# Kernel tuning notes

Hardware: AMD Instinct MI355X
Metric: run time of the kernel (lower is better)

## Reference

```python
import jax, jax.numpy as jnp
import numpy as np

N_NODES = 50000
N_EDGES = 800000
DIMS = [128, 512, 256, 128]
EPS = 1e-5


def setup_inputs() -> dict:
    key = jax.random.key(0)
    ks = jax.random.split(key, 2 + 5 * 3)
    inp = {
        "x": jax.random.normal(ks[0], (N_NODES, DIMS[0]), dtype=jnp.float32),
        "edge_index": jax.random.randint(ks[1], (2, N_EDGES), 0, N_NODES, dtype=jnp.int64),
    }
    ki = 2
    for i in range(3):
        din, dout = DIMS[i], DIMS[i + 1]
        s = 1.0 / np.sqrt(din)
        inp[f"Wl{i}"] = jax.random.uniform(ks[ki + 0], (din, dout), jnp.float32, -s, s)
        inp[f"bl{i}"] = jax.random.uniform(ks[ki + 1], (dout,), jnp.float32, -s, s)
        inp[f"Wr{i}"] = jax.random.uniform(ks[ki + 2], (din, dout), jnp.float32, -s, s)
        inp[f"g{i}"] = jnp.ones((dout,), jnp.float32)
        inp[f"b{i}"] = jnp.zeros((dout,), jnp.float32)
        ki += 5
    return inp


def _sage_mean(x, src, dst, Wl, bl, Wr):
    n = x.shape[0]
    agg = jax.ops.segment_sum(x[src], dst, num_segments=n)  # [N, din]
    deg = jax.ops.segment_sum(jnp.ones((src.shape[0],), x.dtype), dst, num_segments=n)
    mean = agg / jnp.maximum(deg, 1.0)[:, None]
    return mean @ Wl + bl + x @ Wr


def _bn(h, gamma, beta):
    m = h.mean(axis=0)
    v = h.var(axis=0)
    return gamma * (h - m) * jax.lax.rsqrt(v + EPS) + beta


def reference(x, edge_index, Wl0, bl0, Wr0, g0, b0, Wl1, bl1, Wr1, g1, b1, Wl2, bl2, Wr2, g2, b2):
    src, dst = edge_index[0], edge_index[1]
    params = [(Wl0, bl0, Wr0, g0, b0), (Wl1, bl1, Wr1, g1, b1), (Wl2, bl2, Wr2, g2, b2)]
    h = x
    for Wl, bl, Wr, g, b in params:
        h = _sage_mean(h, src, dst, Wl, bl, Wr)
        h = _bn(h, g, b)
        h = jax.nn.relu(h)
        # dropout: identity in eval mode
    return h
```

## Files before the change

### kernel.cpp

```cpp
#include <hip/hip_runtime.h>
#include <cstdint>
#include <cstddef>


#define EPS_BN 1e-5f

typedef unsigned short ushort_t;
typedef __attribute__((ext_vector_type(8))) short short8;
typedef __attribute__((ext_vector_type(4))) float float4v;
typedef __attribute__((ext_vector_type(2))) float float2v;
typedef __attribute__((ext_vector_type(2))) unsigned int uint2v;
typedef __attribute__((ext_vector_type(4))) unsigned int uint4v;

__device__ __forceinline__ float bflo(unsigned int w) {
    union { unsigned int i; float f; } v; v.i = w << 16; return v.f;
}
__device__ __forceinline__ float bfhi(unsigned int w) {
    union { unsigned int i; float f; } v; v.i = w & 0xffff0000u; return v.f;
}
__device__ __forceinline__ ushort_t f2bf(float f) {
    union { float f; unsigned int i; } v; v.f = f;
    unsigned int r = v.i + 0x7fffu + ((v.i >> 16) & 1u);
    return (ushort_t)(r >> 16);
}

__device__ __forceinline__ void async_copy16(void* lds, const void* g) {
    __builtin_amdgcn_global_load_lds(
        (const __attribute__((address_space(1))) unsigned int*)g,
        (__attribute__((address_space(3))) unsigned int*)lds, 16, 0, 0);
}

__device__ __forceinline__ void edge_sd(const int* __restrict__ p, int e, int ne,
                                        bool is64, int& s, int& d) {
    if (is64) { s = p[2 * e];  d = p[2 * ne + 2 * e]; }
    else      { s = p[e];      d = p[ne + e]; }
}
__device__ __forceinline__ int edge_d(const int* __restrict__ p, int e, int ne, bool is64) {
    return is64 ? p[2 * ne + 2 * e] : p[ne + e];
}

__device__ __forceinline__ bool detect_is64(const int* __restrict__ edges,
                                            int* sh_flag, int t) {
    if (t == 0) *sh_flag = 1;
    __syncthreads();
    if (t < 64 && edges[2 * t + 1] != 0) *sh_flag = 0;
    __syncthreads();
    return *sh_flag != 0;
}

#define EPB 2048

__global__ __launch_bounds__(256) void bhist_kernel(
    const int* __restrict__ edges, int ne, int* __restrict__ gcnt) {
    __shared__ int h[256];
    __shared__ int f64;
    int t = threadIdx.x;
    bool is64 = detect_is64(edges, &f64, t);
    h[t] = 0;
    __syncthreads();
    int base_e = blockIdx.x * EPB;
    #pragma unroll
    for (int u = 0; u < EPB / 256; ++u) {
        int i = base_e + u * 256 + t;
        if (i < ne) atomicAdd(&h[edge_d(edges, i, ne, is64) >> 8], 1);
    }
    __syncthreads();
    if (h[t]) atomicAdd(&gcnt[t], h[t]);
}

__global__ __launch_bounds__(256) void bscan_kernel(
    const int* __restrict__ gcnt, int nb, int ne,
    int* __restrict__ bbase, int* __restrict__ bcur) {
    __shared__ int sh[256];
    int t = threadIdx.x;
    int v = (t < nb) ? gcnt[t] : 0;
    sh[t] = v;
    __syncthreads();
    for (int o = 1; o < 256; o <<= 1) {
        int x = (t >= o) ? sh[t - o] : 0;
        __syncthreads();
        sh[t] += x;
        __syncthreads();
    }
    int excl = sh[t] - v;
    if (t < nb) { bbase[t] = excl; bcur[t] = excl; }
    if (t == nb) bbase[t] = ne;
    if (t == 0 && nb == 256) bbase[256] = ne;
}

__global__ __launch_bounds__(256) void bscatter_kernel(
    const int* __restrict__ edges, int ne,
    int* __restrict__ bcur, int* __restrict__ packed) {
    __shared__ int h[256];
    __shared__ int chunkb[256];
    __shared__ int lcur[256];
    __shared__ int f64;
    int t = threadIdx.x;
    bool is64 = detect_is64(edges, &f64, t);
    h[t] = 0;
    lcur[t] = 0;
    __syncthreads();
    int base_e = blockIdx.x * EPB;
    int ent[EPB / 256], eb[EPB / 256];
    #pragma unroll
    for (int u = 0; u < EPB / 256; ++u) {
        int i = base_e + u * 256 + t;
        if (i < ne) {
            int s, d;
            edge_sd(edges, i, ne, is64, s, d);
            ent[u] = s | ((d & 255) << 24);
            eb[u] = d >> 8;
            atomicAdd(&h[eb[u]], 1);
        } else eb[u] = -1;
    }
    __syncthreads();
    if (h[t]) chunkb[t] = atomicAdd(&bcur[t], h[t]);
    __syncthreads();
    #pragma unroll
    for (int u = 0; u < EPB / 256; ++u) {
        if (eb[u] >= 0) {
            int lp = atomicAdd(&lcur[eb[u]], 1);
            packed[chunkb[eb[u]] + lp] = ent[u];
        }
    }
}

__global__ __launch_bounds__(256) void bbuild_kernel(
    const int* __restrict__ packed, const int* __restrict__ bbase,
    int* __restrict__ rowptr, int* __restrict__ csr_src, int n) {
    __shared__ int h[256];
    __shared__ int cur[256];
    int t = threadIdx.x;
    int bb = blockIdx.x;
    int base = bbase[bb], cnt = bbase[bb + 1] - base;
    h[t] = 0;
    __syncthreads();
    for (int i = t; i < cnt; i += 256)
        atomicAdd(&h[(unsigned)packed[base + i] >> 24], 1);
    __syncthreads();
    int v = h[t];
    for (int o = 1; o < 256; o <<= 1) {
        int x = (t >= o) ? h[t - o] : 0;
        __syncthreads();
        h[t] += x;
        __syncthreads();
    }
    int excl = h[t] - v;
    int node = bb * 256 + t;
    if (node <= n) rowptr[node] = base + excl;
    cur[t] = excl;
    __syncthreads();
    for (int i = t; i < cnt; i += 256) {
        int e = packed[base + i];
        int lp = atomicAdd(&cur[(unsigned)e >> 24], 1);
        csr_src[base + lp] = e & 0xffffff;
    }
}

__global__ void prep_all_kernel(
    const float* __restrict__ x, ushort_t* __restrict__ xb, int nxb,
    const float* __restrict__ Wl0, const float* __restrict__ Wr0,
    ushort_t* __restrict__ WT0, int nb0,
    const float* __restrict__ Wl1, const float* __restrict__ Wr1,
    ushort_t* __restrict__ WT1c, int nb1,
    const float* __restrict__ Wl2, const float* __restrict__ Wr2,
    ushort_t* __restrict__ WT2c) {
    const int D0 = 128, D1 = 512, D2 = 256, D3 = 128;
    int b = blockIdx.x;
    if (b < nxb) {
        int i = b * 256 + threadIdx.x;
        xb[i] = f2bf(x[i]);
        return;
    }
    b -= nxb;
    if (b < nb0) {
        int idx = b * 256 + threadIdx.x;
        int K2 = 2 * D0;
        int nn = idx / K2, k = idx - nn * K2;
        float v = (k < D0) ? Wl0[(size_t)k * D1 + nn] : Wr0[(size_t)(k - D0) * D1 + nn];
        WT0[idx] = f2bf(v);
        return;
    }
    b -= nb0;
    if (b < nb1) {
        int idx = b * 256 + threadIdx.x;
        int nn = idx / D1, k = idx - nn * D1;
        float v = (nn < D2) ? Wl1[(size_t)k * D2 + nn] : Wr1[(size_t)k * D2 + (nn - D2)];
        WT1c[idx] = f2bf(v);
        return;
    }
    b -= nb1;
    {
        int idx = b * 256 + threadIdx.x;
        int nn = idx / D2, k = idx - nn * D2;
        float v = (nn < D3) ? Wl2[(size_t)k * D3 + nn] : Wr2[(size_t)k * D3 + (nn - D3)];
        WT2c[idx] = f2bf(v);
    }
}

template <int VEC> struct VecT;
template <> struct VecT<2> { using T = unsigned int; };
template <> struct VecT<4> { using T = uint2v; };
template <> struct VecT<8> { using T = uint4v; };

template <int VEC>
__device__ __forceinline__ void vunpack(typename VecT<VEC>::T v, unsigned int* w) {
    if constexpr (VEC == 2) { w[0] = v; }
    else if constexpr (VEC == 4) { w[0] = v.x; w[1] = v.y; }
    else { w[0] = v.x; w[1] = v.y; w[2] = v.z; w[3] = v.w; }
}

template <int VEC>
__device__ __forceinline__ void vaccum(typename VecT<VEC>::T v, float* acc) {
    unsigned int w[VEC / 2];
    vunpack<VEC>(v, w);
    #pragma unroll
    for (int i = 0; i < VEC / 2; ++i) {
        acc[2 * i + 0] += bflo(w[i]);
        acc[2 * i + 1] += bfhi(w[i]);
    }
}

template <int VEC>
__device__ __forceinline__ void gather_sum(
    const ushort_t* __restrict__ base, const int* __restrict__ csr_src,
    int e0, int e1, int rstride, float* acc) {
    using VT = typename VecT<VEC>::T;
    int e = e0;
    for (; e + 16 <= e1; e += 16) {
        VT v[16];
        #pragma unroll
        for (int u = 0; u < 16; ++u)
            v[u] = *(const VT*)(base + (size_t)csr_src[e + u] * rstride);
        #pragma unroll
        for (int u = 0; u < 16; ++u) vaccum<VEC>(v[u], acc);
    }
    if (e + 8 <= e1) {
        VT v[8];
        #pragma unroll
        for (int u = 0; u < 8; ++u)
            v[u] = *(const VT*)(base + (size_t)csr_src[e + u] * rstride);
        #pragma unroll
        for (int u = 0; u < 8; ++u) vaccum<VEC>(v[u], acc);
        e += 8;
    }
    if (e + 4 <= e1) {
        VT v[4];
        #pragma unroll
        for (int u = 0; u < 4; ++u)
            v[u] = *(const VT*)(base + (size_t)csr_src[e + u] * rstride);
        #pragma unroll
        for (int u = 0; u < 4; ++u) vaccum<VEC>(v[u], acc);
        e += 4;
    }
    if (e + 2 <= e1) {
        VT v0 = *(const VT*)(base + (size_t)csr_src[e] * rstride);
        VT v1 = *(const VT*)(base + (size_t)csr_src[e + 1] * rstride);
        vaccum<VEC>(v0, acc); vaccum<VEC>(v1, acc);
        e += 2;
    }
    if (e < e1)
        vaccum<VEC>(*(const VT*)(base + (size_t)csr_src[e] * rstride), acc);
}

template <int VEC>
__global__ __launch_bounds__(256) void aggregate_wave_kernel(
    const ushort_t* __restrict__ h, ushort_t* __restrict__ mean,
    const int* __restrict__ rowptr, const int* __restrict__ csr_src, int nnodes) {
    const int din = VEC * 64;
    const int wave = threadIdx.x >> 6;
    const int lane = threadIdx.x & 63;
    const int wstride = gridDim.x * 4;
    using VT = typename VecT<VEC>::T;
    for (int wid = blockIdx.x * 4 + wave; wid < nnodes; wid += wstride) {
        int e0 = rowptr[wid], e1 = rowptr[wid + 1];
        float acc[VEC];
        #pragma unroll
        for (int i = 0; i < VEC; ++i) acc[i] = 0.f;
        gather_sum<VEC>(h + (size_t)lane * VEC, csr_src, e0, e1, din, acc);

        int deg = e1 - e0;
        float scale = 1.0f / (float)(deg > 1 ? deg : 1);
        unsigned int o[VEC / 2];
        #pragma unroll
        for (int i = 0; i < VEC / 2; ++i)
            o[i] = (unsigned int)f2bf(acc[2 * i] * scale) |
                   ((unsigned int)f2bf(acc[2 * i + 1] * scale) << 16);
        VT ov;
        if constexpr (VEC == 2) { ov = o[0]; }
        else if constexpr (VEC == 4) { ov.x = o[0]; ov.y = o[1]; }
        else { ov.x = o[0]; ov.y = o[1]; ov.z = o[2]; ov.w = o[3]; }
        *(VT*)(mean + (size_t)wid * din + (size_t)lane * VEC) = ov;
    }
}

template <int VEC>
__global__ __launch_bounds__(256) void aggregate_add_kernel(
    const ushort_t* __restrict__ PR, const float* __restrict__ bias,
    ushort_t* __restrict__ pre,
    const int* __restrict__ rowptr, const int* __restrict__ csr_src, int nnodes,
    float* __restrict__ gsum, float* __restrict__ gsq) {
    const int D = VEC * 64;
    const int stride = 2 * D;
    __shared__ float s_red[2][4][VEC * 64];
    const int wave = threadIdx.x >> 6;
    const int lane = threadIdx.x & 63;
    const int wstride = gridDim.x * 4;
    using VT = typename VecT<VEC>::T;

    float ssum[VEC], ssq[VEC];
    #pragma unroll
    for (int i = 0; i < VEC; ++i) { ssum[i] = 0.f; ssq[i] = 0.f; }

    for (int wid = blockIdx.x * 4 + wave; wid < nnodes; wid += wstride) {
        int e0 = rowptr[wid], e1 = rowptr[wid + 1];
        float acc[VEC];
        #pragma unroll
        for (int i = 0; i < VEC; ++i) acc[i] = 0.f;
        gather_sum<VEC>(PR + (size_t)lane * VEC, csr_src, e0, e1, stride, acc);

        int deg = e1 - e0;
        float scale = 1.0f / (float)(deg > 1 ? deg : 1);

        VT rv = *(const VT*)(PR + (size_t)wid * stride + D + (size_t)lane * VEC);
        unsigned int rw[VEC / 2];
        vunpack<VEC>(rv, rw);
        float o[VEC];
        #pragma unroll
        for (int i = 0; i < VEC / 2; ++i) {
            o[2 * i + 0] = bflo(rw[i]);
            o[2 * i + 1] = bfhi(rw[i]);
        }
        #pragma unroll
        for (int i = 0; i < VEC; ++i) {
            o[i] += acc[i] * scale + bias[lane * VEC + i];
            ssum[i] += o[i];
            ssq[i] += o[i] * o[i];
        }

        unsigned int ow[VEC / 2];
        #pragma unroll
        for (int i = 0; i < VEC / 2; ++i)
            ow[i] = (unsigned int)f2bf(o[2 * i]) | ((unsigned int)f2bf(o[2 * i + 1]) << 16);
        VT ov;
        if constexpr (VEC == 2) { ov = ow[0]; }
        else if constexpr (VEC == 4) { ov.x = ow[0]; ov.y = ow[1]; }
        else { ov.x = ow[0]; ov.y = ow[1]; ov.z = ow[2]; ov.w = ow[3]; }
        *(VT*)(pre + (size_t)wid * D + (size_t)lane * VEC) = ov;
    }

    #pragma unroll
    for (int i = 0; i < VEC; ++i) {
        s_red[0][wave][lane * VEC + i] = ssum[i];
        s_red[1][wave][lane * VEC + i] = ssq[i];
    }
    __syncthreads();
    int t = threadIdx.x;
    if (t < D) {
        float a = s_red[0][0][t] + s_red[0][1][t] + s_red[0][2][t] + s_red[0][3][t];
        float q = s_red[1][0][t] + s_red[1][1][t] + s_red[1][2][t] + s_red[1][3][t];
        atomicAdd(&gsum[t], a);
        atomicAdd(&gsq[t], q);
    }
}

template <bool DUAL, bool BIAS, bool STATS>
__global__ __launch_bounds__(256, 4) void gemm_glds_kernel(
    const ushort_t* __restrict__ A1, const ushort_t* __restrict__ A2,
    const ushort_t* __restrict__ BT, const float* __restrict__ bias,
    ushort_t* __restrict__ Cb, int N, int K1, int Ktot, int Wtot, int nxShift,
    float* __restrict__ gsum, float* __restrict__ gsq) {
    __shared__ ushort_t As[2 * 128 * 32];
    __shared__ ushort_t Bs[2 * 128 * 32];

    const int tid = threadIdx.x;
    const int wave = tid >> 6;
    const int lane = tid & 63;
    const int quad = lane >> 4;
    const int l15 = lane & 15;
    const int sw3 = l15 & 3;

    const int nwg = gridDim.x;
    const int q = nwg >> 3, rr = nwg & 7;
    const int o = blockIdx.x;
    const int xcd = o & 7, sub = o >> 3;
    const int wgid = (xcd < rr ? xcd * (q + 1) : rr * (q + 1) + (xcd - rr) * q) + sub;
    const int bx = wgid & ((1 << nxShift) - 1);
    const int by = wgid >> nxShift;

    const int rowBase = by * 128;
    const int colBase = bx * 128;
    const int wm = (wave >> 1) * 64;
    const int wn = (wave & 1) * 64;

    float4v acc[4][4];
    #pragma unroll
    for (int i = 0; i < 4; ++i)
        #pragma unroll
        for (int j = 0; j < 4; ++j)
            acc[i][j] = (float4v){0.f, 0.f, 0.f, 0.f};

    const int nkt = Ktot / 32;
    const int khalf = K1 / 32;

    auto stage = [&](int buf, int kt) {
        const ushort_t* Asrc = A1;
        int kg = kt * 32;
        if (DUAL && kt >= khalf) { Asrc = A2; kg = (kt - khalf) * 32; }
        const int kb = kt * 32;
        #pragma unroll
        for (int u = 0; u < 2; ++u) {
            int c = u * 256 + tid;
            int r = c >> 2, cc = c & 3;
            int off = (cc ^ (r & 3)) * 8;
            int grow = rowBase + r;
            if (grow >= N) grow = N - 1;
            async_copy16(&As[buf * 4096 + c * 8], Asrc + (size_t)grow * K1 + kg + off);
        }
        #pragma unroll
        for (int u = 0; u < 2; ++u) {
            int c = u * 256 + tid;
            int r = c >> 2, cc = c & 3;
            int off = (cc ^ (r & 3)) * 8;
            async_copy16(&Bs[buf * 4096 + c * 8], BT + (size_t)(colBase + r) * Ktot + kb + off);
        }
    };

    stage(0, 0);
    int cur = 0;
    for (int kt = 0; kt < nkt; ++kt) {
        if (kt + 1 < nkt) {
            stage(cur ^ 1, kt + 1);
            asm volatile("s_waitcnt vmcnt(4)\n\ts_barrier" ::: "memory");
        } else {
            asm volatile("s_waitcnt vmcnt(0)\n\ts_barrier" ::: "memory");
        }

        short8 af[4], bf4[4];
        #pragma unroll
        for (int i = 0; i < 4; ++i)
            af[i] = *(const short8*)&As[cur * 4096 + (wm + i * 16 + l15) * 32 + (quad ^ sw3) * 8];
        #pragma unroll
        for (int j = 0; j < 4; ++j)
            bf4[j] = *(const short8*)&Bs[cur * 4096 + (wn + j * 16 + l15) * 32 + (quad ^ sw3) * 8];
        __builtin_amdgcn_s_setprio(1);
        #pragma unroll
        for (int i = 0; i < 4; ++i)
            #pragma unroll
            for (int j = 0; j < 4; ++j)
                acc[i][j] = __builtin_amdgcn_mfma_f32_16x16x32_bf16(bf4[j], af[i], acc[i][j], 0, 0, 0);
        __builtin_amdgcn_s_setprio(0);
        asm volatile("s_barrier" ::: "memory");
        cur ^= 1;
    }

    float cs[4][4], cq[4][4];
    if constexpr (STATS) {
        #pragma unroll
        for (int j = 0; j < 4; ++j)
            #pragma unroll
            for (int r = 0; r < 4; ++r) { cs[j][r] = 0.f; cq[j][r] = 0.f; }
    }

    ushort_t* lws = &As[wave * 2048];
    #pragma unroll
    for (int p = 0; p < 2; ++p) {
        #pragma unroll
        for (int jj = 0; jj < 2; ++jj) {
            int j = 2 * p + jj;
            float4 bv = make_float4(0.f, 0.f, 0.f, 0.f);
            if (BIAS) bv = *(const float4*)(bias + colBase + wn + j * 16 + quad * 4);
            #pragma unroll
            for (int i = 0; i < 4; ++i) {
                float v0 = acc[i][j][0] + bv.x;
                float v1 = acc[i][j][1] + bv.y;
                float v2 = acc[i][j][2] + bv.z;
                float v3 = acc[i][j][3] + bv.w;
                if constexpr (STATS) {
                    if (rowBase + wm + i * 16 + l15 < N) {
                        cs[j][0] += v0; cq[j][0] += v0 * v0;
                        cs[j][1] += v1; cq[j][1] += v1 * v1;
                        cs[j][2] += v2; cq[j][2] += v2 * v2;
                        cs[j][3] += v3; cq[j][3] += v3 * v3;
                    }
                }
                uint2 pk;
                pk.x = (unsigned int)f2bf(v0) | ((unsigned int)f2bf(v1) << 16);
                pk.y = (unsigned int)f2bf(v2) | ((unsigned int)f2bf(v3) << 16);
                *(uint2*)&lws[(i * 16 + l15) * 32 + jj * 16 + quad * 4] = pk;
            }
        }
        __syncthreads();
        #pragma unroll
        for (int it = 0; it < 4; ++it) {
            int c = it * 64 + lane;
            int row = c >> 2, coff = (c & 3) * 8;
            int grow = rowBase + wm + row;
            if (grow < N) {
                uint4 v = *(const uint4*)&lws[row * 32 + coff];
                *(uint4*)(Cb + (size_t)grow * Wtot + colBase + wn + p * 32 + coff) = v;
            }
        }
        __syncthreads();
    }

    if constexpr (STATS) {
        #pragma unroll
        for (int j = 0; j < 4; ++j)
            #pragma unroll
            for (int r = 0; r < 4; ++r) {
                #pragma unroll
                for (int m = 1; m < 16; m <<= 1) {
                    cs[j][r] += __shfl_xor(cs[j][r], m);
                    cq[j][r] += __shfl_xor(cq[j][r], m);
                }
            }
        if (l15 == 0) {
            #pragma unroll
            for (int j = 0; j < 4; ++j)
                #pragma unroll
                for (int r = 0; r < 4; ++r) {
                    int col = colBase + wn + j * 16 + quad * 4 + r;
                    atomicAdd(&gsum[col], cs[j][r]);
                    atomicAdd(&gsq[col], cq[j][r]);
                }
        }
    }
}

__global__ void bn_relu_b2b_kernel(const ushort_t* __restrict__ h, ushort_t* __restrict__ hb,
                                   int N, int D,
                                   const float* __restrict__ sum, const float* __restrict__ sumsq,
                                   const float* __restrict__ g, const float* __restrict__ b) {
    size_t idx = (size_t)blockIdx.x * blockDim.x + threadIdx.x;
    size_t tot = (size_t)N * D / 2;
    if (idx >= tot) return;
    int cp = (int)(idx & (size_t)(D / 2 - 1));
    int c0 = cp * 2, c1 = c0 + 1;
    float m0 = sum[c0] / (float)N, m1 = sum[c1] / (float)N;
    float i0 = rsqrtf(sumsq[c0] / (float)N - m0 * m0 + EPS_BN);
    float i1 = rsqrtf(sumsq[c1] / (float)N - m1 * m1 + EPS_BN);
    unsigned int w = ((const unsigned int*)h)[idx];
    float v0 = g[c0] * (bflo(w) - m0) * i0 + b[c0];
    float v1 = g[c1] * (bfhi(w) - m1) * i1 + b[c1];
    v0 = v0 > 0.f ? v0 : 0.f;
    v1 = v1 > 0.f ? v1 : 0.f;
    ((unsigned int*)hb)[idx] = (unsigned int)f2bf(v0) | ((unsigned int)f2bf(v1) << 16);
}

__global__ void bn_relu_b2f_kernel(const ushort_t* __restrict__ h, float* __restrict__ hf,
                                   int N, int D,
                                   const float* __restrict__ sum, const float* __restrict__ sumsq,
                                   const float* __restrict__ g, const float* __restrict__ b) {
    size_t idx = (size_t)blockIdx.x * blockDim.x + threadIdx.x;
    size_t tot = (size_t)N * D / 2;
    if (idx >= tot) return;
    int cp = (int)(idx & (size_t)(D / 2 - 1));
    int c0 = cp * 2, c1 = c0 + 1;
    float m0 = sum[c0] / (float)N, m1 = sum[c1] / (float)N;
    float i0 = rsqrtf(sumsq[c0] / (float)N - m0 * m0 + EPS_BN);
    float i1 = rsqrtf(sumsq[c1] / (float)N - m1 * m1 + EPS_BN);
    unsigned int w = ((const unsigned int*)h)[idx];
    float v0 = g[c0] * (bflo(w) - m0) * i0 + b[c0];
    float v1 = g[c1] * (bfhi(w) - m1) * i1 + b[c1];
    float2v o;
    o.x = v0 > 0.f ? v0 : 0.f;
    o.y = v1 > 0.f ? v1 : 0.f;
    *(float2v*)(hf + idx * 2) = o;
}

extern "C" void kernel_launch(void* const* d_in, const int* in_sizes, int n_in,
                              void* d_out, int out_size, void* d_ws, size_t ws_size,
                              hipStream_t stream) {
    const float* x     = (const float*)d_in[0];
    const int*   edges = (const int*)d_in[1];
    const float* Wl0 = (const float*)d_in[2];
    const float* bl0 = (const float*)d_in[3];
    const float* Wr0 = (const float*)d_in[4];
    const float* g0  = (const float*)d_in[5];
    const float* b0  = (const float*)d_in[6];
    const float* Wl1 = (const float*)d_in[7];
    const float* bl1 = (const float*)d_in[8];
    const float* Wr1 = (const float*)d_in[9];
    const float* g1  = (const float*)d_in[10];
    const float* b1  = (const float*)d_in[11];
    const float* Wl2 = (const float*)d_in[12];
    const float* bl2 = (const float*)d_in[13];
    const float* Wr2 = (const float*)d_in[14];
    const float* g2  = (const float*)d_in[15];
    const float* b2  = (const float*)d_in[16];

    const int D0 = 128, D1 = 512, D2 = 256, D3 = 128;
    const int n  = in_sizes[0] / D0;
    const int ne = in_sizes[1] / 2;
    const int NB = (n + 255) >> 8;

    char* base = (char*)d_ws;
    size_t off = 0;
    auto alloc = [&](size_t bytes) -> char* {
        char* p = base + off;
        off = (off + bytes + 255) & ~(size_t)255;
        return p;
    };
    int*      gcnt    = (int*)alloc(256 * 4);
    float*    stats   = (float*)alloc(6 * 512 * 4);
    size_t    zero_span = off;
    int*      bbase   = (int*)alloc(257 * 4);
    int*      bcur    = (int*)alloc(256 * 4);
    int*      packed  = (int*)alloc((size_t)ne * 4);
    int*      rowptr  = (int*)alloc((size_t)(n + 1) * 4);
    int*      csr_src = (int*)alloc((size_t)ne * 4);
    ushort_t* xb      = (ushort_t*)alloc((size_t)n * D0 * 2);
    ushort_t* mb      = (ushort_t*)alloc((size_t)n * 512 * 2);
    ushort_t* h1b     = (ushort_t*)alloc((size_t)n * D1 * 2);
    ushort_t* h2b     = (ushort_t*)alloc((size_t)n * D2 * 2);
    ushort_t* hpre    = (ushort_t*)alloc((size_t)n * 512 * 2);
    ushort_t* WT0     = (ushort_t*)alloc((size_t)D1 * 2 * D0 * 2);
    ushort_t* WT1c    = (ushort_t*)alloc((size_t)(2 * D2) * D1 * 2);
    ushort_t* WT2c    = (ushort_t*)alloc((size_t)(2 * D3) * D2 * 2);
    float*    out     = (float*)d_out;
    (void)ws_size; (void)n_in; (void)out_size;

    hipMemsetAsync(base, 0, zero_span, stream);

    int ablk = (ne + EPB - 1) / EPB;
    bhist_kernel<<<ablk, 256, 0, stream>>>(edges, ne, gcnt);
    bscan_kernel<<<1, 256, 0, stream>>>(gcnt, NB, ne, bbase, bcur);
    bscatter_kernel<<<ablk, 256, 0, stream>>>(edges, ne, bcur, packed);
    bbuild_kernel<<<NB, 256, 0, stream>>>(packed, bbase, rowptr, csr_src, n);

    const int nxb = (n * D0) / 256;
    const int nb0 = (D1 * 2 * D0) / 256;
    const int nb1 = (2 * D2 * D1) / 256;
    const int nb2 = (2 * D3 * D2) / 256;
    prep_all_kernel<<<nxb + nb0 + nb1 + nb2, 256, 0, stream>>>(
        x, xb, nxb, Wl0, Wr0, WT0, nb0, Wl1, Wr1, WT1c, nb1, Wl2, Wr2, WT2c);

    const int aggGrid = 2048;
    const int rowBlocks = (n + 127) / 128;
    float* st0 = stats + 0 * 1024;
    float* st1 = stats + 1 * 1024;
    float* st2 = stats + 2 * 1024;

    aggregate_wave_kernel<2><<<aggGrid, 256, 0, stream>>>(xb, mb, rowptr, csr_src, n);
    gemm_glds_kernel<true, true, true><<<4 * rowBlocks, 256, 0, stream>>>(
        mb, xb, WT0, bl0, hpre, n, D0, 2 * D0, D1, 2, st0, st0 + 512);
    bn_relu_b2b_kernel<<<((size_t)n * D1 / 2 + 255) / 256, 256, 0, stream>>>(
        hpre, h1b, n, D1, st0, st0 + 512, g0, b0);

    gemm_glds_kernel<false, false, false><<<4 * rowBlocks, 256, 0, stream>>>(
        h1b, nullptr, WT1c, nullptr, mb, n, D1, D1, 2 * D2, 2, nullptr, nullptr);
    aggregate_add_kernel<4><<<aggGrid, 256, 0, stream>>>(
        mb, bl1, hpre, rowptr, csr_src, n, st1, st1 + 512);
    bn_relu_b2b_kernel<<<((size_t)n * D2 / 2 + 255) / 256, 256, 0, stream>>>(
        hpre, h2b, n, D2, st1, st1 + 512, g1, b1);

    gemm_glds_kernel<false, false, false><<<2 * rowBlocks, 256, 0, stream>>>(
        h2b, nullptr, WT2c, nullptr, mb, n, D2, D2, 2 * D3, 1, nullptr, nullptr);
    aggregate_add_kernel<2><<<aggGrid, 256, 0, stream>>>(
        mb, bl2, hpre, rowptr, csr_src, n, st2, st2 + 512);
    bn_relu_b2f_kernel<<<((size_t)n * D3 / 2 + 255) / 256, 256, 0, stream>>>(
        hpre, out, n, D3, st2, st2 + 512, g2, b2);
}
```

Baseline: 570.9 us.

## Keep weight panel resident in LDS and stream A fragments from global

Replaces the double-buffered 128x128 LDS GEMM with a persistent-style kernel. Each workgroup loads a full K x COLS weight panel into LDS once, then loops over row tiles, reading A fragments directly from global memory into registers. Epilogue writes bf16 results straight to global without an LDS transpose stage. This removes per-k-tile barriers and repeated B staging, at the cost of unhidden global latency on A loads, larger LDS use, and a fixed grid of 512 workgroups.

```diff
diff --git a/kernel.cpp b/kernel.cpp
--- a/kernel.cpp
+++ b/kernel.cpp
@@ -364,110 +364,105 @@
     }
 }
 
-template <bool DUAL, bool BIAS, bool STATS>
-__global__ __launch_bounds__(256, 4) void gemm_glds_kernel(
+template <int K, int COLS, bool DUAL, bool BIAS, bool STATS>
+__global__ __launch_bounds__(256, 2) void gemm_bres_kernel(
     const ushort_t* __restrict__ A1, const ushort_t* __restrict__ A2,
     const ushort_t* __restrict__ BT, const float* __restrict__ bias,
-    ushort_t* __restrict__ Cb, int N, int K1, int Ktot, int Wtot, int nxShift,
-    float* __restrict__ gsum, float* __restrict__ gsq) {
-    __shared__ ushort_t As[2 * 128 * 32];
-    __shared__ ushort_t Bs[2 * 128 * 32];
+    ushort_t* __restrict__ Cb, int N, int nRowTiles, int RG, int panelsLog2,
+    int Wtot, float* __restrict__ gsum, float* __restrict__ gsq) {
+    __shared__ ushort_t Bs[COLS * K];
 
     const int tid = threadIdx.x;
     const int wave = tid >> 6;
     const int lane = tid & 63;
     const int quad = lane >> 4;
     const int l15 = lane & 15;
-    const int sw3 = l15 & 3;
 
     const int nwg = gridDim.x;
     const int q = nwg >> 3, rr = nwg & 7;
     const int o = blockIdx.x;
     const int xcd = o & 7, sub = o >> 3;
     const int wgid = (xcd < rr ? xcd * (q + 1) : rr * (q + 1) + (xcd - rr) * q) + sub;
-    const int bx = wgid & ((1 << nxShift) - 1);
-    const int by = wgid >> nxShift;
-
-    const int rowBase = by * 128;
-    const int colBase = bx * 128;
+    const int panel = wgid & ((1 << panelsLog2) - 1);
+    const int rowGroup = wgid >> panelsLog2;
+    const int colBase = panel * COLS;
+
+    constexpr int CPC = K / 8;
+    constexpr int CPT = COLS * CPC / 256;
+    #pragma unroll
+    for (int u = 0; u < CPT; ++u) {
+        int c = u * 256 + tid;
+        int col = c / CPC, cc = c - col * CPC;
+        int scc = cc ^ (col & 7);
+        async_copy16(&Bs[c * 8], BT + (size_t)(colBase + col) * K + scc * 8);
+    }
+    __syncthreads();
+
     const int wm = (wave >> 1) * 64;
-    const int wn = (wave & 1) * 64;
-
-    float4v acc[4][4];
-    #pragma unroll
-    for (int i = 0; i < 4; ++i)
-        #pragma unroll
-        for (int j = 0; j < 4; ++j)
-            acc[i][j] = (float4v){0.f, 0.f, 0.f, 0.f};
-
-    const int nkt = Ktot / 32;
-    const int khalf = K1 / 32;
-
-    auto stage = [&](int buf, int kt) {
-        const ushort_t* Asrc = A1;
-        int kg = kt * 32;
-        if (DUAL && kt >= khalf) { Asrc = A2; kg = (kt - khalf) * 32; }
-        const int kb = kt * 32;
-        #pragma unroll
-        for (int u = 0; u < 2; ++u) {
-            int c = u * 256 + tid;
-            int r = c >> 2, cc = c & 3;
-            int off = (cc ^ (r & 3)) * 8;
-            int grow = rowBase + r;
+    constexpr int WN = COLS / 2;
+    const int wn = (wave & 1) * WN;
+    constexpr int NJ = WN / 16;
+    constexpr int NKK = K / 32;
+    constexpr int AS = DUAL ? K / 2 : K;
+
+    float cs[NJ][4], cq[NJ][4];
+    if constexpr (STATS) {
+        #pragma unroll
+        for (int j = 0; j < NJ; ++j)
+            #pragma unroll
+            for (int r = 0; r < 4; ++r) { cs[j][r] = 0.f; cq[j][r] = 0.f; }
+    }
+
+    for (int rt = rowGroup; rt < nRowTiles; rt += RG) {
+        const int rowBase = rt * 128;
+        const ushort_t* ap[4];
+        const ushort_t* ap2[4];
+        int growv[4];
+        #pragma unroll
+        for (int i = 0; i < 4; ++i) {
+            int grow = rowBase + wm + i * 16 + l15;
+            growv[i] = grow;
             if (grow >= N) grow = N - 1;
-            async_copy16(&As[buf * 4096 + c * 8], Asrc + (size_t)grow * K1 + kg + off);
+            ap[i] = A1 + (size_t)grow * AS + quad * 8;
+            if (DUAL) ap2[i] = A2 + (size_t)grow * AS + quad * 8;
         }
-        #pragma unroll
-        for (int u = 0; u < 2; ++u) {
-            int c = u * 256 + tid;
-            int r = c >> 2, cc = c & 3;
-            int off = (cc ^ (r & 3)) * 8;
-            async_copy16(&Bs[buf * 4096 + c * 8], BT + (size_t)(colBase + r) * Ktot + kb + off);
+
+        float4v acc[4][NJ];
+        #pragma unroll
+        for (int i = 0; i < 4; ++i)
+            #pragma unroll
+            for (int j = 0; j < NJ; ++j)
+                acc[i][j] = (float4v){0.f, 0.f, 0.f, 0.f};
+
+        #pragma unroll
+        for (int kk = 0; kk < NKK; ++kk) {
+            short8 af[4], bf[NJ];
+            #pragma unroll
+            for (int i = 0; i < 4; ++i) {
+                if constexpr (DUAL) {
+                    if (kk < NKK / 2) af[i] = *(const short8*)(ap[i] + kk * 32);
+                    else              af[i] = *(const short8*)(ap2[i] + (kk - NKK / 2) * 32);
+                } else {
+                    af[i] = *(const short8*)(ap[i] + kk * 32);
+                }
+            }
+            #pragma unroll
+            for (int j = 0; j < NJ; ++j) {
+                int col = wn + j * 16 + l15;
+                int ct = (kk * 4 + quad) ^ (col & 7);
+                bf[j] = *(const short8*)&Bs[col * K + ct * 8];
+            }
+            __builtin_amdgcn_s_setprio(1);
+            #pragma unroll
+            for (int i = 0; i < 4; ++i)
+                #pragma unroll
+                for (int j = 0; j < NJ; ++j)
+                    acc[i][j] = __builtin_amdgcn_mfma_f32_16x16x32_bf16(bf[j], af[i], acc[i][j], 0, 0, 0);
+            __builtin_amdgcn_s_setprio(0);
         }
-    };
-
-    stage(0, 0);
-    int cur = 0;
-    for (int kt = 0; kt < nkt; ++kt) {
-        if (kt + 1 < nkt) {
-            stage(cur ^ 1, kt + 1);
-            asm volatile("s_waitcnt vmcnt(4)\n\ts_barrier" ::: "memory");
-        } else {
-            asm volatile("s_waitcnt vmcnt(0)\n\ts_barrier" ::: "memory");
-        }
-
-        short8 af[4], bf4[4];
-        #pragma unroll
-        for (int i = 0; i < 4; ++i)
-            af[i] = *(const short8*)&As[cur * 4096 + (wm + i * 16 + l15) * 32 + (quad ^ sw3) * 8];
-        #pragma unroll
-        for (int j = 0; j < 4; ++j)
-            bf4[j] = *(const short8*)&Bs[cur * 4096 + (wn + j * 16 + l15) * 32 + (quad ^ sw3) * 8];
-        __builtin_amdgcn_s_setprio(1);
-        #pragma unroll
-        for (int i = 0; i < 4; ++i)
-            #pragma unroll
-            for (int j = 0; j < 4; ++j)
-                acc[i][j] = __builtin_amdgcn_mfma_f32_16x16x32_bf16(bf4[j], af[i], acc[i][j], 0, 0, 0);
-        __builtin_amdgcn_s_setprio(0);
-        asm volatile("s_barrier" ::: "memory");
-        cur ^= 1;
-    }
-
-    float cs[4][4], cq[4][4];
-    if constexpr (STATS) {
-        #pragma unroll
-        for (int j = 0; j < 4; ++j)
-            #pragma unroll
-            for (int r = 0; r < 4; ++r) { cs[j][r] = 0.f; cq[j][r] = 0.f; }
-    }
-
-    ushort_t* lws = &As[wave * 2048];
-    #pragma unroll
-    for (int p = 0; p < 2; ++p) {
-        #pragma unroll
-        for (int jj = 0; jj < 2; ++jj) {
-            int j = 2 * p + jj;
+
+        #pragma unroll
+        for (int j = 0; j < NJ; ++j) {
             float4 bv = make_float4(0.f, 0.f, 0.f, 0.f);
             if (BIAS) bv = *(const float4*)(bias + colBase + wn + j * 16 + quad * 4);
             #pragma unroll
@@ -476,37 +471,25 @@
                 float v1 = acc[i][j][1] + bv.y;
                 float v2 = acc[i][j][2] + bv.z;
                 float v3 = acc[i][j][3] + bv.w;
-                if constexpr (STATS) {
-                    if (rowBase + wm + i * 16 + l15 < N) {
+                if (growv[i] < N) {
+                    if constexpr (STATS) {
                         cs[j][0] += v0; cq[j][0] += v0 * v0;
                         cs[j][1] += v1; cq[j][1] += v1 * v1;
                         cs[j][2] += v2; cq[j][2] += v2 * v2;
                         cs[j][3] += v3; cq[j][3] += v3 * v3;
                     }
+                    uint2v pk;
+                    pk.x = (unsigned int)f2bf(v0) | ((unsigned int)f2bf(v1) << 16);
+                    pk.y = (unsigned int)f2bf(v2) | ((unsigned int)f2bf(v3) << 16);
+                    *(uint2v*)(Cb + (size_t)growv[i] * Wtot + colBase + wn + j * 16 + quad * 4) = pk;
                 }
-                uint2 pk;
-                pk.x = (unsigned int)f2bf(v0) | ((unsigned int)f2bf(v1) << 16);
-                pk.y = (unsigned int)f2bf(v2) | ((unsigned int)f2bf(v3) << 16);
-                *(uint2*)&lws[(i * 16 + l15) * 32 + jj * 16 + quad * 4] = pk;
             }
         }
-        __syncthreads();
-        #pragma unroll
-        for (int it = 0; it < 4; ++it) {
-            int c = it * 64 + lane;
-            int row = c >> 2, coff = (c & 3) * 8;
-            int grow = rowBase + wm + row;
-            if (grow < N) {
-                uint4 v = *(const uint4*)&lws[row * 32 + coff];
-                *(uint4*)(Cb + (size_t)grow * Wtot + colBase + wn + p * 32 + coff) = v;
-            }
-        }
-        __syncthreads();
     }
 
     if constexpr (STATS) {
         #pragma unroll
-        for (int j = 0; j < 4; ++j)
+        for (int j = 0; j < NJ; ++j)
             #pragma unroll
             for (int r = 0; r < 4; ++r) {
                 #pragma unroll
@@ -517,7 +500,7 @@
             }
         if (l15 == 0) {
             #pragma unroll
-            for (int j = 0; j < 4; ++j)
+            for (int j = 0; j < NJ; ++j)
                 #pragma unroll
                 for (int r = 0; r < 4; ++r) {
                     int col = colBase + wn + j * 16 + quad * 4 + r;
@@ -637,26 +620,26 @@
         x, xb, nxb, Wl0, Wr0, WT0, nb0, Wl1, Wr1, WT1c, nb1, Wl2, Wr2, WT2c);
 
     const int aggGrid = 2048;
-    const int rowBlocks = (n + 127) / 128;
+    const int rowTiles = (n + 127) / 128;
     float* st0 = stats + 0 * 1024;
     float* st1 = stats + 1 * 1024;
     float* st2 = stats + 2 * 1024;
 
     aggregate_wave_kernel<2><<<aggGrid, 256, 0, stream>>>(xb, mb, rowptr, csr_src, n);
-    gemm_glds_kernel<true, true, true><<<4 * rowBlocks, 256, 0, stream>>>(
-        mb, xb, WT0, bl0, hpre, n, D0, 2 * D0, D1, 2, st0, st0 + 512);
+    gemm_bres_kernel<256, 128, true, true, true><<<512, 256, 0, stream>>>(
+        mb, xb, WT0, bl0, hpre, n, rowTiles, 128, 2, D1, st0, st0 + 512);
     bn_relu_b2b_kernel<<<((size_t)n * D1 / 2 + 255) / 256, 256, 0, stream>>>(
         hpre, h1b, n, D1, st0, st0 + 512, g0, b0);
 
-    gemm_glds_kernel<false, false, false><<<4 * rowBlocks, 256, 0, stream>>>(
-        h1b, nullptr, WT1c, nullptr, mb, n, D1, D1, 2 * D2, 2, nullptr, nullptr);
+    gemm_bres_kernel<512, 64, false, false, false><<<512, 256, 0, stream>>>(
+        h1b, nullptr, WT1c, nullptr, mb, n, rowTiles, 64, 3, 2 * D2, nullptr, nullptr);
     aggregate_add_kernel<4><<<aggGrid, 256, 0, stream>>>(
         mb, bl1, hpre, rowptr, csr_src, n, st1, st1 + 512);
     bn_relu_b2b_kernel<<<((size_t)n * D2 / 2 + 255) / 256, 256, 0, stream>>>(
         hpre, h2b, n, D2, st1, st1 + 512, g1, b1);
 
-    gemm_glds_kernel<false, false, false><<<2 * rowBlocks, 256, 0, stream>>>(
-        h2b, nullptr, WT2c, nullptr, mb, n, D2, D2, 2 * D3, 1, nullptr, nullptr);
+    gemm_bres_kernel<256, 128, false, false, false><<<512, 256, 0, stream>>>(
+        h2b, nullptr, WT2c, nullptr, mb, n, rowTiles, 256, 1, 2 * D3, nullptr, nullptr);
     aggregate_add_kernel<2><<<aggGrid, 256, 0, stream>>>(
         mb, bl2, hpre, rowptr, csr_src, n, st2, st2 + 512);
     bn_relu_b2f_kernel<<<((size_t)n * D3 / 2 + 255) / 256, 256, 0, stream>>>(
```

Result: slower. 604.7 us (+5.9%).

## Fuse BatchNorm+ReLU into next GEMM's A-operand load path

Applied to the files above, without the earlier changes.

Drops the standalone bf16 BN+ReLU kernels for layers 0 and 1. Each following GEMM now reads the pre-activation buffer directly, computes per-channel scale/shift in LDS from the accumulated stats, and applies the affine transform and ReLU to A fragments after loading them from LDS. This removes a full read and write of the intermediate activations, two kernel launches and the h1b/h2b buffers. In exchange, the elementwise work is repeated for every column block and adds VALU work inside the MFMA loop.

```diff
diff --git a/kernel.cpp b/kernel.cpp
--- a/kernel.cpp
+++ b/kernel.cpp
@@ -364,14 +364,18 @@
     }
 }
 
-template <bool DUAL, bool BIAS, bool STATS>
+template <bool DUAL, bool BIAS, bool STATS, bool BNA>
 __global__ __launch_bounds__(256, 4) void gemm_glds_kernel(
     const ushort_t* __restrict__ A1, const ushort_t* __restrict__ A2,
     const ushort_t* __restrict__ BT, const float* __restrict__ bias,
     ushort_t* __restrict__ Cb, int N, int K1, int Ktot, int Wtot, int nxShift,
-    float* __restrict__ gsum, float* __restrict__ gsq) {
+    float* __restrict__ gsum, float* __restrict__ gsq,
+    const float* __restrict__ bsum, const float* __restrict__ bsq,
+    const float* __restrict__ bng, const float* __restrict__ bnb) {
     __shared__ ushort_t As[2 * 128 * 32];
     __shared__ ushort_t Bs[2 * 128 * 32];
+    __shared__ float bnsc[BNA ? 512 : 1];
+    __shared__ float bnsh[BNA ? 512 : 1];
 
     const int tid = threadIdx.x;
     const int wave = tid >> 6;
@@ -392,6 +396,17 @@
     const int colBase = bx * 128;
     const int wm = (wave >> 1) * 64;
     const int wn = (wave & 1) * 64;
+
+    if constexpr (BNA) {
+        for (int t = tid; t < K1; t += 256) {
+            float m = bsum[t] / (float)N;
+            float inv = rsqrtf(bsq[t] / (float)N - m * m + EPS_BN);
+            float sc = bng[t] * inv;
+            bnsc[t] = sc;
+            bnsh[t] = bnb[t] - m * sc;
+        }
+        __syncthreads();
+    }
 
     float4v acc[4][4];
     #pragma unroll
@@ -443,6 +458,24 @@
         #pragma unroll
         for (int j = 0; j < 4; ++j)
             bf4[j] = *(const short8*)&Bs[cur * 4096 + (wn + j * 16 + l15) * 32 + (quad ^ sw3) * 8];
+
+        if constexpr (BNA) {
+            int k0 = kt * 32 + quad * 8;
+            #pragma unroll
+            for (int e = 0; e < 8; ++e) {
+                float sc = bnsc[k0 + e];
+                float sh = bnsh[k0 + e];
+                #pragma unroll
+                for (int i = 0; i < 4; ++i) {
+                    unsigned int u = ((unsigned int)(unsigned short)af[i][e]) << 16;
+                    union { unsigned int w; float f; } cv; cv.w = u;
+                    float v = cv.f * sc + sh;
+                    v = v > 0.f ? v : 0.f;
+                    af[i][e] = (short)f2bf(v);
+                }
+            }
+        }
+
         __builtin_amdgcn_s_setprio(1);
         #pragma unroll
         for (int i = 0; i < 4; ++i)
@@ -528,26 +561,6 @@
     }
 }
 
-__global__ void bn_relu_b2b_kernel(const ushort_t* __restrict__ h, ushort_t* __restrict__ hb,
-                                   int N, int D,
-                                   const float* __restrict__ sum, const float* __restrict__ sumsq,
-                                   const float* __restrict__ g, const float* __restrict__ b) {
-    size_t idx = (size_t)blockIdx.x * blockDim.x + threadIdx.x;
-    size_t tot = (size_t)N * D / 2;
-    if (idx >= tot) return;
-    int cp = (int)(idx & (size_t)(D / 2 - 1));
-    int c0 = cp * 2, c1 = c0 + 1;
-    float m0 = sum[c0] / (float)N, m1 = sum[c1] / (float)N;
-    float i0 = rsqrtf(sumsq[c0] / (float)N - m0 * m0 + EPS_BN);
-    float i1 = rsqrtf(sumsq[c1] / (float)N - m1 * m1 + EPS_BN);
-    unsigned int w = ((const unsigned int*)h)[idx];
-    float v0 = g[c0] * (bflo(w) - m0) * i0 + b[c0];
-    float v1 = g[c1] * (bfhi(w) - m1) * i1 + b[c1];
-    v0 = v0 > 0.f ? v0 : 0.f;
-    v1 = v1 > 0.f ? v1 : 0.f;
-    ((unsigned int*)hb)[idx] = (unsigned int)f2bf(v0) | ((unsigned int)f2bf(v1) << 16);
-}
-
 __global__ void bn_relu_b2f_kernel(const ushort_t* __restrict__ h, float* __restrict__ hf,
                                    int N, int D,
                                    const float* __restrict__ sum, const float* __restrict__ sumsq,
@@ -612,8 +625,6 @@
     int*      csr_src = (int*)alloc((size_t)ne * 4);
     ushort_t* xb      = (ushort_t*)alloc((size_t)n * D0 * 2);
     ushort_t* mb      = (ushort_t*)alloc((size_t)n * 512 * 2);
-    ushort_t* h1b     = (ushort_t*)alloc((size_t)n * D1 * 2);
-    ushort_t* h2b     = (ushort_t*)alloc((size_t)n * D2 * 2);
     ushort_t* hpre    = (ushort_t*)alloc((size_t)n * 512 * 2);
     ushort_t* WT0     = (ushort_t*)alloc((size_t)D1 * 2 * D0 * 2);
     ushort_t* WT1c    = (ushort_t*)alloc((size_t)(2 * D2) * D1 * 2);
@@ -643,20 +654,19 @@
     float* st2 = stats + 2 * 1024;
 
     aggregate_wave_kernel<2><<<aggGrid, 256, 0, stream>>>(xb, mb, rowptr, csr_src, n);
-    gemm_glds_kernel<true, true, true><<<4 * rowBlocks, 256, 0, stream>>>(
-        mb, xb, WT0, bl0, hpre, n, D0, 2 * D0, D1, 2, st0, st0 + 512);
-    bn_relu_b2b_kernel<<<((size_t)n * D1 / 2 + 255) / 256, 256, 0, stream>>>(
-        hpre, h1b, n, D1, st0, st0 + 512, g0, b0);
-
-    gemm_glds_kernel<false, false, false><<<4 * rowBlocks, 256, 0, stream>>>(
-        h1b, nullptr, WT1c, nullptr, mb, n, D1, D1, 2 * D2, 2, nullptr, nullptr);
+    gemm_glds_kernel<true, true, true, false><<<4 * rowBlocks, 256, 0, stream>>>(
+        mb, xb, WT0, bl0, hpre, n, D0, 2 * D0, D1, 2, st0, st0 + 512,
+        nullptr, nullptr, nullptr, nullptr);
+
+    gemm_glds_kernel<false, false, false, true><<<4 * rowBlocks, 256, 0, stream>>>(
+        hpre, nullptr, WT1c, nullptr, mb, n, D1, D1, 2 * D2, 2, nullptr, nullptr,
+        st0, st0 + 512, g0, b0);
     aggregate_add_kernel<4><<<aggGrid, 256, 0, stream>>>(
         mb, bl1, hpre, rowptr, csr_src, n, st1, st1 + 512);
-    bn_relu_b2b_kernel<<<((size_t)n * D2 / 2 + 255) / 256, 256, 0, stream>>>(
-        hpre, h2b, n, D2, st1, st1 + 512, g1, b1);
-
-    gemm_glds_kernel<false, false, false><<<2 * rowBlocks, 256, 0, stream>>>(
-        h2b, nullptr, WT2c, nullptr, mb, n, D2, D2, 2 * D3, 1, nullptr, nullptr);
+
+    gemm_glds_kernel<false, false, false, true><<<2 * rowBlocks, 256, 0, stream>>>(
+        hpre, nullptr, WT2c, nullptr, mb, n, D2, D2, 2 * D3, 1, nullptr, nullptr,
+        st1, st1 + 512, g1, b1);
     aggregate_add_kernel<2><<<aggGrid, 256, 0, stream>>>(
         mb, bl2, hpre, rowptr, csr_src, n, st2, st2 + 512);
     bn_relu_b2f_kernel<<<((size_t)n * D3 / 2 + 255) / 256, 256, 0, stream>>>(
```

New measurement: 568.6 us. No clear change (-0.4%).
